# Optimization experiments

Measured on AMD Instinct MI355X. Metric: run time of the kernel, lower is better.

The kernel has to match this reference:

```python
import jax, jax.numpy as jnp
import numpy as np

B, T, D_IN, H, NH, R = 32, 1024, 64, 128, 4, 3
HD = H // NH  # 32


def _p(key, shape, scale=0.02):
    return jax.random.normal(key, shape, dtype=jnp.float32) * scale


def setup_inputs() -> dict:
    key = jax.random.key(0)
    ks = jax.random.split(key, 8)
    return {
        "x": jax.random.normal(ks[0], (B, T, D_IN), dtype=jnp.float32),
        "theta_w": _p(ks[1], (H, D_IN)),
        "theta_b": jnp.zeros((H,), jnp.float32),
        "in_proj_w": _p(ks[2], (3 * H, H)),
        "in_proj_b": jnp.zeros((3 * H,), jnp.float32),
        "out_proj_w": _p(ks[3], (H, H)),
        "out_proj_b": jnp.zeros((H,), jnp.float32),
        "ln_g": jnp.ones((H,), jnp.float32),
        "ln_b": jnp.zeros((H,), jnp.float32),
        "w1": _p(ks[4], (H, H)),
        "b1": jnp.zeros((H,), jnp.float32),
        "w2": _p(ks[5], (2, H)),
        "b2": jnp.zeros((2,), jnp.float32),
    }


def _build_adj(t, radius):
    # banded adjacency: adj[i,j] = 1/(1+|i-j|) for |i-j| <= radius, row-normalized
    idx = jnp.arange(t)
    d = jnp.abs(idx[:, None] - idx[None, :])
    adj = jnp.where(d <= radius, 1.0 / (1.0 + d.astype(jnp.float32)), 0.0)
    return adj / jnp.clip(adj.sum(axis=1, keepdims=True), 1e-8)


def reference(x, theta_w, theta_b, in_proj_w, in_proj_b, out_proj_w, out_proj_b,
              ln_g, ln_b, w1, b1, w2, b2):
    h = x @ theta_w.T + theta_b                       # [B,T,H]
    adj = _build_adj(T, R)                            # [T,T]
    g = jnp.einsum('ij,bjh->bih', adj, h)             # banded temporal aggregation

    # torch nn.MultiheadAttention (batch_first, eval -> no dropout)
    qkv = g @ in_proj_w.T + in_proj_b                 # [B,T,3H]
    q, k, v = jnp.split(qkv, 3, axis=-1)
    split_heads = lambda t: t.reshape(B, T, NH, HD).transpose(0, 2, 1, 3)
    q, k, v = split_heads(q), split_heads(k), split_heads(v)
    scores = jnp.einsum('bntd,bnsd->bnts', q, k) / jnp.sqrt(jnp.float32(HD))
    attn = jax.nn.softmax(scores, axis=-1)
    o = jnp.einsum('bnts,bnsd->bntd', attn, v)
    o = o.transpose(0, 2, 1, 3).reshape(B, T, H)
    a = o @ out_proj_w.T + out_proj_b                 # [B,T,H]

    # head on last timestep: LayerNorm -> Linear -> GELU(exact) -> Linear
    last = a[:, -1, :]                                # [B,H]
    mu = last.mean(-1, keepdims=True)
    var = ((last - mu) ** 2).mean(-1, keepdims=True)
    ln = (last - mu) / jnp.sqrt(var + 1e-5) * ln_g + ln_b
    hid = jax.nn.gelu(ln @ w1.T + b1, approximate=False)
    return hid @ w2.T + b2                            # [B,2]
```

## Files before the change

kernel.cpp:

```cpp
#include <hip/hip_runtime.h>
#include <math.h>

#define TT 1024

__global__ __launch_bounds__(256) void k_qr(
    const float* __restrict__ x, const float* __restrict__ theta_w,
    const float* __restrict__ theta_b, const float* __restrict__ ipw,
    const float* __restrict__ ipb, float* __restrict__ r_out) {
  const int b = blockIdx.x;
  const int tid = threadIdx.x;
  __shared__ float s_xs[64];
  __shared__ float s_y[128];
  __shared__ float s_q[128];
  __shared__ float s_z[4][128];
  const float* __restrict__ xb = x + (size_t)b * TT * 64;

  if (tid < 64) {
    float acc = xb[(TT - 1) * 64 + tid]
              + 0.5f        * xb[(TT - 2) * 64 + tid]
              + (1.f / 3.f) * xb[(TT - 3) * 64 + tid]
              + 0.25f       * xb[(TT - 4) * 64 + tid];
    s_xs[tid] = acc * (12.f / 25.f);
  }
  __syncthreads();
  if (tid < 128) {
    const float* tr = theta_w + tid * 64;
    float acc = theta_b[tid];
    for (int d = 0; d < 64; ++d) acc += tr[d] * s_xs[d];
    s_y[tid] = acc;
  }
  __syncthreads();
  {
    const int g = tid >> 4, l = tid & 15;
    for (int pass = 0; pass < 8; ++pass) {
      const int e = pass * 16 + g;
      const float* wr = ipw + e * 128 + l * 8;
      float acc = 0.f;
      #pragma unroll
      for (int u = 0; u < 8; ++u) acc += wr[u] * s_y[l * 8 + u];
      acc += __shfl_xor(acc, 1);
      acc += __shfl_xor(acc, 2);
      acc += __shfl_xor(acc, 4);
      acc += __shfl_xor(acc, 8);
      if (l == 0) s_q[e] = acc + ipb[e];
    }
  }
  __syncthreads();
  for (int rep = 0; rep < 2; ++rep) {
    const int idx = tid + rep * 256;
    const int n = idx >> 7, c = idx & 127;
    const float* qn = &s_q[n * 32];
    float acc = 0.f;
    for (int e = 0; e < 32; ++e) acc += ipw[(128 + n * 32 + e) * 128 + c] * qn[e];
    s_z[n][c] = acc;
  }
  __syncthreads();
  {
    const int n = tid >> 6, d = tid & 63;
    const float* zn = s_z[n];
    float acc = 0.f;
    for (int c = 0; c < 128; ++c) acc += theta_w[c * 64 + d] * zn[c];
    r_out[(b * 4 + n) * 64 + d] = acc * 0.17677669529663687f;
  }
}

__global__ __launch_bounds__(256) void k_t(
    const float* __restrict__ x, const float* __restrict__ r_in,
    float* __restrict__ t_out) {
  const int b = blockIdx.x >> 4;
  const int chunk = blockIdx.x & 15;
  const int tid = threadIdx.x;
  __shared__ __align__(16) float s_r[256];
  s_r[tid] = r_in[b * 256 + tid];
  __syncthreads();
  const int g = tid >> 4, l = tid & 15;
  const float4 r0 = ((const float4*)(s_r +   0))[l];
  const float4 r1 = ((const float4*)(s_r +  64))[l];
  const float4 r2 = ((const float4*)(s_r + 128))[l];
  const float4 r3 = ((const float4*)(s_r + 192))[l];
  const float* __restrict__ xb = x + ((size_t)b * TT + chunk * 64) * 64;
  for (int it = 0; it < 4; ++it) {
    const int jj = it * 16 + g;
    const float4 xv = ((const float4*)(xb + jj * 64))[l];
    float p0 = xv.x * r0.x + xv.y * r0.y + xv.z * r0.z + xv.w * r0.w;
    float p1 = xv.x * r1.x + xv.y * r1.y + xv.z * r1.z + xv.w * r1.w;
    float p2 = xv.x * r2.x + xv.y * r2.y + xv.z * r2.z + xv.w * r2.w;
    float p3 = xv.x * r3.x + xv.y * r3.y + xv.z * r3.z + xv.w * r3.w;
    #pragma unroll
    for (int m = 1; m <= 8; m <<= 1) {
      p0 += __shfl_xor(p0, m);
      p1 += __shfl_xor(p1, m);
      p2 += __shfl_xor(p2, m);
      p3 += __shfl_xor(p3, m);
    }
    if (l == 0) {
      const int j = chunk * 64 + jj;
      t_out[(b * 4 + 0) * TT + j] = p0;
      t_out[(b * 4 + 1) * TT + j] = p1;
      t_out[(b * 4 + 2) * TT + j] = p2;
      t_out[(b * 4 + 3) * TT + j] = p3;
    }
  }
}

__global__ __launch_bounds__(256) void k_sm(float* __restrict__ t_pt) {
  const int bn = blockIdx.x;
  const int tid = threadIdx.x;
  __shared__ __align__(16) float s_t[TT];
  __shared__ float s_p[TT];
  __shared__ float s_red[4];
  ((float4*)s_t)[tid] = ((const float4*)(t_pt + bn * TT))[tid];
  __syncthreads();

  float sc[4], wsv[4];
  float lmax = -1e30f;
  const int s0 = tid * 4;
  for (int k = 0; k < 4; ++k) {
    const int s = s0 + k;
    float acc = 0.f, wsum = 0.f;
    #pragma unroll
    for (int dj = -3; dj <= 3; ++dj) {
      const int j = s + dj;
      if (j >= 0 && j < TT) {
        const float w = 1.f / (1.f + (float)(dj < 0 ? -dj : dj));
        acc += w * s_t[j];
        wsum += w;
      }
    }
    sc[k] = acc / wsum;
    wsv[k] = wsum;
    lmax = fmaxf(lmax, sc[k]);
  }
  #pragma unroll
  for (int m = 32; m >= 1; m >>= 1) lmax = fmaxf(lmax, __shfl_xor(lmax, m));
  if ((tid & 63) == 0) s_red[tid >> 6] = lmax;
  __syncthreads();
  const float bmax = fmaxf(fmaxf(s_red[0], s_red[1]), fmaxf(s_red[2], s_red[3]));
  __syncthreads();
  float lsum = 0.f;
  for (int k = 0; k < 4; ++k) {
    const float e = expf(sc[k] - bmax);
    lsum += e;
    s_p[s0 + k] = e / wsv[k];
  }
  #pragma unroll
  for (int m = 32; m >= 1; m >>= 1) lsum += __shfl_xor(lsum, m);
  if ((tid & 63) == 0) s_red[tid >> 6] = lsum;
  __syncthreads();
  const float inv_denom = 1.f / (s_red[0] + s_red[1] + s_red[2] + s_red[3]);
  for (int k = 0; k < 4; ++k) {
    const int j = s0 + k;
    float acc = 0.f;
    #pragma unroll
    for (int dj = -3; dj <= 3; ++dj) {
      const int s = j + dj;
      if (s >= 0 && s < TT)
        acc += (1.f / (1.f + (float)(dj < 0 ? -dj : dj))) * s_p[s];
    }
    t_pt[bn * TT + j] = acc * inv_denom;
  }
}

__global__ __launch_bounds__(256) void k_u(
    const float* __restrict__ x, const float* __restrict__ pt_in,
    float* __restrict__ up_out) {
  const int b = blockIdx.x >> 4;
  const int chunk = blockIdx.x & 15;
  const int tid = threadIdx.x;
  __shared__ __align__(16) float s_x[64][64];
  __shared__ float s_p[4][64];
  const float* __restrict__ xb = x + ((size_t)b * TT + chunk * 64) * 64;
  #pragma unroll
  for (int it = 0; it < 4; ++it) {
    const int i4 = tid + it * 256;
    ((float4*)&s_x[0][0])[i4] = ((const float4*)xb)[i4];
  }
  {
    const int n = tid >> 6, jj = tid & 63;
    s_p[n][jj] = pt_in[(b * 4 + n) * TT + chunk * 64 + jj];
  }
  __syncthreads();
  const int n = tid >> 6, d = tid & 63;
  float acc = 0.f;
  for (int jj = 0; jj < 64; ++jj) acc += s_p[n][jj] * s_x[jj][d];
  up_out[((b * 16 + chunk) * 4 + n) * 64 + d] = acc;
}

__global__ __launch_bounds__(128) void k_tail(
    const float* __restrict__ up_in, const float* __restrict__ theta_w,
    const float* __restrict__ theta_b, const float* __restrict__ ipw,
    const float* __restrict__ ipb, const float* __restrict__ Wout,
    const float* __restrict__ outb, const float* __restrict__ ln_g,
    const float* __restrict__ ln_b, const float* __restrict__ w1,
    const float* __restrict__ b1, const float* __restrict__ w2,
    const float* __restrict__ b2, float* __restrict__ out) {
  const int b = blockIdx.x;
  const int tid = threadIdx.x;
  __shared__ float s_u[256];
  __shared__ float s_w[4][128];
  __shared__ float s_o[128], s_ln[128], s_hid[128], s_red[2];

  for (int rep = 0; rep < 2; ++rep) {
    const int idx = tid + rep * 128;
    float acc = 0.f;
    for (int c = 0; c < 16; ++c) acc += up_in[(b * 16 + c) * 256 + idx];
    s_u[idx] = acc;
  }
  __syncthreads();
  for (int rep = 0; rep < 4; ++rep) {
    const int idx = tid + rep * 128;
    const int n = idx >> 7, c = idx & 127;
    const float* tr = theta_w + c * 64;
    const float* un = &s_u[n * 64];
    float acc = theta_b[c];
    for (int d = 0; d < 64; ++d) acc += tr[d] * un[d];
    s_w[n][c] = acc;
  }
  __syncthreads();
  {
    const int e = tid, n = e >> 5;
    const float* wr = ipw + (256 + e) * 128;
    const float* wn = s_w[n];
    float acc = ipb[256 + e];
    for (int c = 0; c < 128; ++c) acc += wr[c] * wn[c];
    s_o[e] = acc;
  }
  __syncthreads();
  const int e = tid;
  float a = outb[e];
  {
    const float* wr = Wout + e * 128;
    for (int f = 0; f < 128; ++f) a += wr[f] * s_o[f];
  }
  float sum = a;
  #pragma unroll
  for (int m = 32; m >= 1; m >>= 1) sum += __shfl_xor(sum, m);
  if ((e & 63) == 0) s_red[e >> 6] = sum;
  __syncthreads();
  const float mu = (s_red[0] + s_red[1]) * (1.f / 128.f);
  __syncthreads();
  const float d = a - mu;
  float sq = d * d;
  #pragma unroll
  for (int m = 32; m >= 1; m >>= 1) sq += __shfl_xor(sq, m);
  if ((e & 63) == 0) s_red[e >> 6] = sq;
  __syncthreads();
  const float var = (s_red[0] + s_red[1]) * (1.f / 128.f);
  const float ln = d / sqrtf(var + 1e-5f) * ln_g[e] + ln_b[e];
  s_ln[e] = ln;
  __syncthreads();
  float h = b1[e];
  {
    const float* w1r = w1 + e * 128;
    for (int f = 0; f < 128; ++f) h += w1r[f] * s_ln[f];
  }
  h = 0.5f * h * (1.f + erff(h * 0.70710678118654752f));
  s_hid[e] = h;
  __syncthreads();
  if (e < 2) {
    float acc = b2[e];
    const float* w2r = w2 + e * 128;
    for (int f = 0; f < 128; ++f) acc += w2r[f] * s_hid[f];
    out[b * 2 + e] = acc;
  }
}

extern "C" void kernel_launch(void* const* d_in, const int* in_sizes, int n_in,
                              void* d_out, int out_size, void* d_ws, size_t ws_size,
                              hipStream_t stream) {
  const float* x       = (const float*)d_in[0];
  const float* theta_w = (const float*)d_in[1];
  const float* theta_b = (const float*)d_in[2];
  const float* ipw     = (const float*)d_in[3];
  const float* ipb     = (const float*)d_in[4];
  const float* outw    = (const float*)d_in[5];
  const float* outb    = (const float*)d_in[6];
  const float* ln_g    = (const float*)d_in[7];
  const float* ln_b    = (const float*)d_in[8];
  const float* w1      = (const float*)d_in[9];
  const float* b1      = (const float*)d_in[10];
  const float* w2      = (const float*)d_in[11];
  const float* b2      = (const float*)d_in[12];

  float* ws = (float*)d_ws;
  float* r  = ws;
  float* t  = ws + 8192;
  float* up = ws + 8192 + 131072;

  k_qr  <<< 32, 256, 0, stream>>>(x, theta_w, theta_b, ipw, ipb, r);
  k_t   <<<512, 256, 0, stream>>>(x, r, t);
  k_sm  <<<128, 256, 0, stream>>>(t);
  k_u   <<<512, 256, 0, stream>>>(x, t, up);
  k_tail<<< 32, 128, 0, stream>>>(up, theta_w, theta_b, ipw, ipb, outw, outb,
                                  ln_g, ln_b, w1, b1, w2, b2, (float*)d_out);
}
```

Measured before the change: 117.9 us.

## Fuse five-stage pipeline into one 1024-thread kernel per batch

Merges the query/r computation, score projection, banded softmax, value aggregation and MLP head into a single kernel with one 1024-thread block per batch, keeping all intermediates in shared memory. This removes four extra launches and the global-memory round trips through the workspace. The trade-off is only 32 blocks across the device, so each batch's 256 KB of x is streamed by a single CU rather than 16. Shared memory use also rises to roughly 60 KB per block.

```diff
diff --git a/kernel.cpp b/kernel.cpp
--- a/kernel.cpp
+++ b/kernel.cpp
@@ -3,191 +3,8 @@
 
 #define TT 1024
 
-__global__ __launch_bounds__(256) void k_qr(
+__global__ __launch_bounds__(1024) void k_fused(
     const float* __restrict__ x, const float* __restrict__ theta_w,
-    const float* __restrict__ theta_b, const float* __restrict__ ipw,
-    const float* __restrict__ ipb, float* __restrict__ r_out) {
-  const int b = blockIdx.x;
-  const int tid = threadIdx.x;
-  __shared__ float s_xs[64];
-  __shared__ float s_y[128];
-  __shared__ float s_q[128];
-  __shared__ float s_z[4][128];
-  const float* __restrict__ xb = x + (size_t)b * TT * 64;
-
-  if (tid < 64) {
-    float acc = xb[(TT - 1) * 64 + tid]
-              + 0.5f        * xb[(TT - 2) * 64 + tid]
-              + (1.f / 3.f) * xb[(TT - 3) * 64 + tid]
-              + 0.25f       * xb[(TT - 4) * 64 + tid];
-    s_xs[tid] = acc * (12.f / 25.f);
-  }
-  __syncthreads();
-  if (tid < 128) {
-    const float* tr = theta_w + tid * 64;
-    float acc = theta_b[tid];
-    for (int d = 0; d < 64; ++d) acc += tr[d] * s_xs[d];
-    s_y[tid] = acc;
-  }
-  __syncthreads();
-  {
-    const int g = tid >> 4, l = tid & 15;
-    for (int pass = 0; pass < 8; ++pass) {
-      const int e = pass * 16 + g;
-      const float* wr = ipw + e * 128 + l * 8;
-      float acc = 0.f;
-      #pragma unroll
-      for (int u = 0; u < 8; ++u) acc += wr[u] * s_y[l * 8 + u];
-      acc += __shfl_xor(acc, 1);
-      acc += __shfl_xor(acc, 2);
-      acc += __shfl_xor(acc, 4);
-      acc += __shfl_xor(acc, 8);
-      if (l == 0) s_q[e] = acc + ipb[e];
-    }
-  }
-  __syncthreads();
-  for (int rep = 0; rep < 2; ++rep) {
-    const int idx = tid + rep * 256;
-    const int n = idx >> 7, c = idx & 127;
-    const float* qn = &s_q[n * 32];
-    float acc = 0.f;
-    for (int e = 0; e < 32; ++e) acc += ipw[(128 + n * 32 + e) * 128 + c] * qn[e];
-    s_z[n][c] = acc;
-  }
-  __syncthreads();
-  {
-    const int n = tid >> 6, d = tid & 63;
-    const float* zn = s_z[n];
-    float acc = 0.f;
-    for (int c = 0; c < 128; ++c) acc += theta_w[c * 64 + d] * zn[c];
-    r_out[(b * 4 + n) * 64 + d] = acc * 0.17677669529663687f;
-  }
-}
-
-__global__ __launch_bounds__(256) void k_t(
-    const float* __restrict__ x, const float* __restrict__ r_in,
-    float* __restrict__ t_out) {
-  const int b = blockIdx.x >> 4;
-  const int chunk = blockIdx.x & 15;
-  const int tid = threadIdx.x;
-  __shared__ __align__(16) float s_r[256];
-  s_r[tid] = r_in[b * 256 + tid];
-  __syncthreads();
-  const int g = tid >> 4, l = tid & 15;
-  const float4 r0 = ((const float4*)(s_r +   0))[l];
-  const float4 r1 = ((const float4*)(s_r +  64))[l];
-  const float4 r2 = ((const float4*)(s_r + 128))[l];
-  const float4 r3 = ((const float4*)(s_r + 192))[l];
-  const float* __restrict__ xb = x + ((size_t)b * TT + chunk * 64) * 64;
-  for (int it = 0; it < 4; ++it) {
-    const int jj = it * 16 + g;
-    const float4 xv = ((const float4*)(xb + jj * 64))[l];
-    float p0 = xv.x * r0.x + xv.y * r0.y + xv.z * r0.z + xv.w * r0.w;
-    float p1 = xv.x * r1.x + xv.y * r1.y + xv.z * r1.z + xv.w * r1.w;
-    float p2 = xv.x * r2.x + xv.y * r2.y + xv.z * r2.z + xv.w * r2.w;
-    float p3 = xv.x * r3.x + xv.y * r3.y + xv.z * r3.z + xv.w * r3.w;
-    #pragma unroll
-    for (int m = 1; m <= 8; m <<= 1) {
-      p0 += __shfl_xor(p0, m);
-      p1 += __shfl_xor(p1, m);
-      p2 += __shfl_xor(p2, m);
-      p3 += __shfl_xor(p3, m);
-    }
-    if (l == 0) {
-      const int j = chunk * 64 + jj;
-      t_out[(b * 4 + 0) * TT + j] = p0;
-      t_out[(b * 4 + 1) * TT + j] = p1;
-      t_out[(b * 4 + 2) * TT + j] = p2;
-      t_out[(b * 4 + 3) * TT + j] = p3;
-    }
-  }
-}
-
-__global__ __launch_bounds__(256) void k_sm(float* __restrict__ t_pt) {
-  const int bn = blockIdx.x;
-  const int tid = threadIdx.x;
-  __shared__ __align__(16) float s_t[TT];
-  __shared__ float s_p[TT];
-  __shared__ float s_red[4];
-  ((float4*)s_t)[tid] = ((const float4*)(t_pt + bn * TT))[tid];
-  __syncthreads();
-
-  float sc[4], wsv[4];
-  float lmax = -1e30f;
-  const int s0 = tid * 4;
-  for (int k = 0; k < 4; ++k) {
-    const int s = s0 + k;
-    float acc = 0.f, wsum = 0.f;
-    #pragma unroll
-    for (int dj = -3; dj <= 3; ++dj) {
-      const int j = s + dj;
-      if (j >= 0 && j < TT) {
-        const float w = 1.f / (1.f + (float)(dj < 0 ? -dj : dj));
-        acc += w * s_t[j];
-        wsum += w;
-      }
-    }
-    sc[k] = acc / wsum;
-    wsv[k] = wsum;
-    lmax = fmaxf(lmax, sc[k]);
-  }
-  #pragma unroll
-  for (int m = 32; m >= 1; m >>= 1) lmax = fmaxf(lmax, __shfl_xor(lmax, m));
-  if ((tid & 63) == 0) s_red[tid >> 6] = lmax;
-  __syncthreads();
-  const float bmax = fmaxf(fmaxf(s_red[0], s_red[1]), fmaxf(s_red[2], s_red[3]));
-  __syncthreads();
-  float lsum = 0.f;
-  for (int k = 0; k < 4; ++k) {
-    const float e = expf(sc[k] - bmax);
-    lsum += e;
-    s_p[s0 + k] = e / wsv[k];
-  }
-  #pragma unroll
-  for (int m = 32; m >= 1; m >>= 1) lsum += __shfl_xor(lsum, m);
-  if ((tid & 63) == 0) s_red[tid >> 6] = lsum;
-  __syncthreads();
-  const float inv_denom = 1.f / (s_red[0] + s_red[1] + s_red[2] + s_red[3]);
-  for (int k = 0; k < 4; ++k) {
-    const int j = s0 + k;
-    float acc = 0.f;
-    #pragma unroll
-    for (int dj = -3; dj <= 3; ++dj) {
-      const int s = j + dj;
-      if (s >= 0 && s < TT)
-        acc += (1.f / (1.f + (float)(dj < 0 ? -dj : dj))) * s_p[s];
-    }
-    t_pt[bn * TT + j] = acc * inv_denom;
-  }
-}
-
-__global__ __launch_bounds__(256) void k_u(
-    const float* __restrict__ x, const float* __restrict__ pt_in,
-    float* __restrict__ up_out) {
-  const int b = blockIdx.x >> 4;
-  const int chunk = blockIdx.x & 15;
-  const int tid = threadIdx.x;
-  __shared__ __align__(16) float s_x[64][64];
-  __shared__ float s_p[4][64];
-  const float* __restrict__ xb = x + ((size_t)b * TT + chunk * 64) * 64;
-  #pragma unroll
-  for (int it = 0; it < 4; ++it) {
-    const int i4 = tid + it * 256;
-    ((float4*)&s_x[0][0])[i4] = ((const float4*)xb)[i4];
-  }
-  {
-    const int n = tid >> 6, jj = tid & 63;
-    s_p[n][jj] = pt_in[(b * 4 + n) * TT + chunk * 64 + jj];
-  }
-  __syncthreads();
-  const int n = tid >> 6, d = tid & 63;
-  float acc = 0.f;
-  for (int jj = 0; jj < 64; ++jj) acc += s_p[n][jj] * s_x[jj][d];
-  up_out[((b * 16 + chunk) * 4 + n) * 64 + d] = acc;
-}
-
-__global__ __launch_bounds__(128) void k_tail(
-    const float* __restrict__ up_in, const float* __restrict__ theta_w,
     const float* __restrict__ theta_b, const float* __restrict__ ipw,
     const float* __restrict__ ipb, const float* __restrict__ Wout,
     const float* __restrict__ outb, const float* __restrict__ ln_g,
@@ -196,20 +13,187 @@
     const float* __restrict__ b2, float* __restrict__ out) {
   const int b = blockIdx.x;
   const int tid = threadIdx.x;
+
+  __shared__ float s_xs[64];
+  __shared__ float s_y[128];
+  __shared__ float s_q[128];
+  __shared__ float s_z[4][128];
+  __shared__ __align__(16) float s_r[256];
+  __shared__ __align__(16) float s_t[4][TT];
+  __shared__ __align__(16) float s_p[4][TT];
+  __shared__ __align__(16) float s_ptT[TT][4];
+  __shared__ float s_up[16][4][64];
   __shared__ float s_u[256];
   __shared__ float s_w[4][128];
-  __shared__ float s_o[128], s_ln[128], s_hid[128], s_red[2];
-
-  for (int rep = 0; rep < 2; ++rep) {
-    const int idx = tid + rep * 128;
+  __shared__ float s_o[128], s_ln[128], s_hid[128];
+  __shared__ float s_red4[4][4];
+  __shared__ float s_red2[2];
+
+  const float* __restrict__ xb = x + (size_t)b * TT * 64;
+
+  if (tid < 64) {
+    float acc = xb[(TT - 1) * 64 + tid]
+              + 0.5f        * xb[(TT - 2) * 64 + tid]
+              + (1.f / 3.f) * xb[(TT - 3) * 64 + tid]
+              + 0.25f       * xb[(TT - 4) * 64 + tid];
+    s_xs[tid] = acc * (12.f / 25.f);
+  }
+  __syncthreads();
+  if (tid < 128) {
+    const float* tr = theta_w + tid * 64;
+    float acc = theta_b[tid];
+    for (int d = 0; d < 64; ++d) acc += tr[d] * s_xs[d];
+    s_y[tid] = acc;
+  }
+  __syncthreads();
+  if (tid < 256) {
+    const int g = tid >> 4, l = tid & 15;
+    for (int pass = 0; pass < 8; ++pass) {
+      const int e = pass * 16 + g;
+      const float* wr = ipw + e * 128 + l * 8;
+      float acc = 0.f;
+      #pragma unroll
+      for (int u = 0; u < 8; ++u) acc += wr[u] * s_y[l * 8 + u];
+      acc += __shfl_xor(acc, 1);
+      acc += __shfl_xor(acc, 2);
+      acc += __shfl_xor(acc, 4);
+      acc += __shfl_xor(acc, 8);
+      if (l == 0) s_q[e] = acc + ipb[e];
+    }
+  }
+  __syncthreads();
+  if (tid < 512) {
+    const int n = tid >> 7, c = tid & 127;
+    const float* qn = &s_q[n * 32];
     float acc = 0.f;
-    for (int c = 0; c < 16; ++c) acc += up_in[(b * 16 + c) * 256 + idx];
-    s_u[idx] = acc;
-  }
-  __syncthreads();
-  for (int rep = 0; rep < 4; ++rep) {
-    const int idx = tid + rep * 128;
-    const int n = idx >> 7, c = idx & 127;
+    for (int e = 0; e < 32; ++e) acc += ipw[(128 + n * 32 + e) * 128 + c] * qn[e];
+    s_z[n][c] = acc;
+  }
+  __syncthreads();
+  if (tid < 256) {
+    const int n = tid >> 6, d = tid & 63;
+    const float* zn = s_z[n];
+    float acc = 0.f;
+    for (int c = 0; c < 128; ++c) acc += theta_w[c * 64 + d] * zn[c];
+    s_r[n * 64 + d] = acc * 0.17677669529663687f;
+  }
+  __syncthreads();
+
+  {
+    const int g = tid >> 4, l = tid & 15;
+    const float4 r0 = ((const float4*)(s_r +   0))[l];
+    const float4 r1 = ((const float4*)(s_r +  64))[l];
+    const float4 r2 = ((const float4*)(s_r + 128))[l];
+    const float4 r3 = ((const float4*)(s_r + 192))[l];
+    for (int it = 0; it < 16; ++it) {
+      const int j = it * 64 + g;
+      const float4 xv = ((const float4*)(xb + j * 64))[l];
+      float p0 = xv.x * r0.x + xv.y * r0.y + xv.z * r0.z + xv.w * r0.w;
+      float p1 = xv.x * r1.x + xv.y * r1.y + xv.z * r1.z + xv.w * r1.w;
+      float p2 = xv.x * r2.x + xv.y * r2.y + xv.z * r2.z + xv.w * r2.w;
+      float p3 = xv.x * r3.x + xv.y * r3.y + xv.z * r3.z + xv.w * r3.w;
+      #pragma unroll
+      for (int m = 1; m <= 8; m <<= 1) {
+        p0 += __shfl_xor(p0, m);
+        p1 += __shfl_xor(p1, m);
+        p2 += __shfl_xor(p2, m);
+        p3 += __shfl_xor(p3, m);
+      }
+      if (l == 0) {
+        s_t[0][j] = p0;
+        s_t[1][j] = p1;
+        s_t[2][j] = p2;
+        s_t[3][j] = p3;
+      }
+    }
+  }
+  __syncthreads();
+
+  {
+    const int hg = tid >> 8, ht = tid & 255;
+    float sc[4], wsv[4];
+    float lmax = -1e30f;
+    #pragma unroll
+    for (int k = 0; k < 4; ++k) {
+      const int s = ht + k * 256;
+      float acc = 0.f, wsum = 0.f;
+      #pragma unroll
+      for (int dj = -3; dj <= 3; ++dj) {
+        const int j = s + dj;
+        if (j >= 0 && j < TT) {
+          const float w = 1.f / (1.f + (float)(dj < 0 ? -dj : dj));
+          acc += w * s_t[hg][j];
+          wsum += w;
+        }
+      }
+      sc[k] = acc / wsum;
+      wsv[k] = wsum;
+      lmax = fmaxf(lmax, sc[k]);
+    }
+    #pragma unroll
+    for (int m = 32; m >= 1; m >>= 1) lmax = fmaxf(lmax, __shfl_xor(lmax, m));
+    if ((ht & 63) == 0) s_red4[hg][ht >> 6] = lmax;
+    __syncthreads();
+    const float bmax = fmaxf(fmaxf(s_red4[hg][0], s_red4[hg][1]),
+                             fmaxf(s_red4[hg][2], s_red4[hg][3]));
+    __syncthreads();
+    float lsum = 0.f;
+    #pragma unroll
+    for (int k = 0; k < 4; ++k) {
+      const float e = expf(sc[k] - bmax);
+      lsum += e;
+      s_p[hg][ht + k * 256] = e / wsv[k];
+    }
+    #pragma unroll
+    for (int m = 32; m >= 1; m >>= 1) lsum += __shfl_xor(lsum, m);
+    if ((ht & 63) == 0) s_red4[hg][ht >> 6] = lsum;
+    __syncthreads();
+    const float inv_denom =
+        1.f / (s_red4[hg][0] + s_red4[hg][1] + s_red4[hg][2] + s_red4[hg][3]);
+    #pragma unroll
+    for (int k = 0; k < 4; ++k) {
+      const int j = ht + k * 256;
+      float acc = 0.f;
+      #pragma unroll
+      for (int dj = -3; dj <= 3; ++dj) {
+        const int s = j + dj;
+        if (s >= 0 && s < TT)
+          acc += (1.f / (1.f + (float)(dj < 0 ? -dj : dj))) * s_p[hg][s];
+      }
+      s_ptT[j][hg] = acc * inv_denom;
+    }
+  }
+  __syncthreads();
+
+  {
+    const int jp = tid >> 6, d = tid & 63;
+    const float* xr = xb + (size_t)(jp * 64) * 64 + d;
+    float a0 = 0.f, a1 = 0.f, a2 = 0.f, a3 = 0.f;
+    for (int jj = 0; jj < 64; ++jj) {
+      const float xv = xr[jj * 64];
+      const int j = jp * 64 + jj;
+      const float4 pv = *(const float4*)(&s_ptT[j][0]);
+      a0 += pv.x * xv;
+      a1 += pv.y * xv;
+      a2 += pv.z * xv;
+      a3 += pv.w * xv;
+    }
+    s_up[jp][0][d] = a0;
+    s_up[jp][1][d] = a1;
+    s_up[jp][2][d] = a2;
+    s_up[jp][3][d] = a3;
+  }
+  __syncthreads();
+  if (tid < 256) {
+    const int n = tid >> 6, d = tid & 63;
+    float acc = 0.f;
+    for (int c = 0; c < 16; ++c) acc += s_up[c][n][d];
+    s_u[n * 64 + d] = acc;
+  }
+  __syncthreads();
+
+  if (tid < 512) {
+    const int n = tid >> 7, c = tid & 127;
     const float* tr = theta_w + c * 64;
     const float* un = &s_u[n * 64];
     float acc = theta_b[c];
@@ -217,7 +201,7 @@
     s_w[n][c] = acc;
   }
   __syncthreads();
-  {
+  if (tid < 128) {
     const int e = tid, n = e >> 5;
     const float* wr = ipw + (256 + e) * 128;
     const float* wn = s_w[n];
@@ -226,42 +210,50 @@
     s_o[e] = acc;
   }
   __syncthreads();
-  const int e = tid;
-  float a = outb[e];
-  {
+  float a_val = 0.f;
+  if (tid < 128) {
+    const int e = tid;
+    a_val = outb[e];
     const float* wr = Wout + e * 128;
-    for (int f = 0; f < 128; ++f) a += wr[f] * s_o[f];
-  }
-  float sum = a;
-  #pragma unroll
-  for (int m = 32; m >= 1; m >>= 1) sum += __shfl_xor(sum, m);
-  if ((e & 63) == 0) s_red[e >> 6] = sum;
-  __syncthreads();
-  const float mu = (s_red[0] + s_red[1]) * (1.f / 128.f);
-  __syncthreads();
-  const float d = a - mu;
-  float sq = d * d;
-  #pragma unroll
-  for (int m = 32; m >= 1; m >>= 1) sq += __shfl_xor(sq, m);
-  if ((e & 63) == 0) s_red[e >> 6] = sq;
-  __syncthreads();
-  const float var = (s_red[0] + s_red[1]) * (1.f / 128.f);
-  const float ln = d / sqrtf(var + 1e-5f) * ln_g[e] + ln_b[e];
-  s_ln[e] = ln;
-  __syncthreads();
-  float h = b1[e];
-  {
+    for (int f = 0; f < 128; ++f) a_val += wr[f] * s_o[f];
+    float sum = a_val;
+    #pragma unroll
+    for (int m = 32; m >= 1; m >>= 1) sum += __shfl_xor(sum, m);
+    if ((e & 63) == 0) s_red2[e >> 6] = sum;
+  }
+  __syncthreads();
+  const float mu = (s_red2[0] + s_red2[1]) * (1.f / 128.f);
+  __syncthreads();
+  if (tid < 128) {
+    const float d = a_val - mu;
+    float sq = d * d;
+    #pragma unroll
+    for (int m = 32; m >= 1; m >>= 1) sq += __shfl_xor(sq, m);
+    if ((tid & 63) == 0) s_red2[tid >> 6] = sq;
+  }
+  __syncthreads();
+  if (tid < 128) {
+    const int e = tid;
+    const float var = (s_red2[0] + s_red2[1]) * (1.f / 128.f);
+    const float d = a_val - mu;
+    const float ln = d / sqrtf(var + 1e-5f) * ln_g[e] + ln_b[e];
+    s_ln[e] = ln;
+  }
+  __syncthreads();
+  if (tid < 128) {
+    const int e = tid;
+    float h = b1[e];
     const float* w1r = w1 + e * 128;
     for (int f = 0; f < 128; ++f) h += w1r[f] * s_ln[f];
-  }
-  h = 0.5f * h * (1.f + erff(h * 0.70710678118654752f));
-  s_hid[e] = h;
-  __syncthreads();
-  if (e < 2) {
-    float acc = b2[e];
-    const float* w2r = w2 + e * 128;
+    h = 0.5f * h * (1.f + erff(h * 0.70710678118654752f));
+    s_hid[e] = h;
+  }
+  __syncthreads();
+  if (tid < 2) {
+    float acc = b2[tid];
+    const float* w2r = w2 + tid * 128;
     for (int f = 0; f < 128; ++f) acc += w2r[f] * s_hid[f];
-    out[b * 2 + e] = acc;
+    out[b * 2 + tid] = acc;
   }
 }
 
@@ -282,15 +274,8 @@
   const float* w2      = (const float*)d_in[11];
   const float* b2      = (const float*)d_in[12];
 
-  float* ws = (float*)d_ws;
-  float* r  = ws;
-  float* t  = ws + 8192;
-  float* up = ws + 8192 + 131072;
-
-  k_qr  <<< 32, 256, 0, stream>>>(x, theta_w, theta_b, ipw, ipb, r);
-  k_t   <<<512, 256, 0, stream>>>(x, r, t);
-  k_sm  <<<128, 256, 0, stream>>>(t);
-  k_u   <<<512, 256, 0, stream>>>(x, t, up);
-  k_tail<<< 32, 128, 0, stream>>>(up, theta_w, theta_b, ipw, ipb, outw, outb,
-                                  ln_g, ln_b, w1, b1, w2, b2, (float*)d_out);
+  (void)d_ws; (void)ws_size;
+
+  k_fused<<<32, 1024, 0, stream>>>(x, theta_w, theta_b, ipw, ipb, outw, outb,
+                                   ln_g, ln_b, w1, b1, w2, b2, (float*)d_out);
 }
```

Measured after the change: 118.2 us. Within noise of the previous version (+0.3%).

## Fuse qr, scoring, softmax and value-aggregation kernels into one per-(batch,head) block

Applied to the files above, without the earlier changes.

Replaces four kernels (k_qr, k_t, k_sm, k_u) with a single 1024-thread kernel, one block per (batch, head). Each block computes its head's query projection, the scores, the banded softmax and the weighted x reduction entirely in shared memory. This removes three launches and the global round-trips for r, t and the partial up sums. In exchange each block re-reads x for its batch (four times per batch overall), recomputes the shared prefix per head, and the grid shrinks to 128 blocks.

```diff
diff --git a/kernel.cpp b/kernel.cpp
--- a/kernel.cpp
+++ b/kernel.cpp
@@ -3,16 +3,26 @@
 
 #define TT 1024
 
-__global__ __launch_bounds__(256) void k_qr(
+__global__ __launch_bounds__(1024) void k_bn(
     const float* __restrict__ x, const float* __restrict__ theta_w,
     const float* __restrict__ theta_b, const float* __restrict__ ipw,
-    const float* __restrict__ ipb, float* __restrict__ r_out) {
-  const int b = blockIdx.x;
+    const float* __restrict__ ipb, float* __restrict__ u_ws) {
+  const int bid = blockIdx.x;
+  const int b = bid & 31;
+  const int n = bid >> 5;
   const int tid = threadIdx.x;
+
   __shared__ float s_xs[64];
   __shared__ float s_y[128];
-  __shared__ float s_q[128];
-  __shared__ float s_z[4][128];
+  __shared__ float s_qn[32];
+  __shared__ float s_z[128];
+  __shared__ __align__(16) float s_r[64];
+  __shared__ __align__(16) float s_t[TT];
+  __shared__ __align__(16) float s_p[TT];
+  __shared__ __align__(16) float s_pt[TT];
+  __shared__ float s_up[16][64];
+  __shared__ float s_red[16];
+
   const float* __restrict__ xb = x + (size_t)b * TT * 64;
 
   if (tid < 64) {
@@ -30,164 +40,113 @@
     s_y[tid] = acc;
   }
   __syncthreads();
-  {
+  if (tid < 512) {
     const int g = tid >> 4, l = tid & 15;
-    for (int pass = 0; pass < 8; ++pass) {
-      const int e = pass * 16 + g;
-      const float* wr = ipw + e * 128 + l * 8;
-      float acc = 0.f;
+    const int e = n * 32 + g;
+    const float* wr = ipw + e * 128 + l * 8;
+    float acc = 0.f;
+    #pragma unroll
+    for (int u = 0; u < 8; ++u) acc += wr[u] * s_y[l * 8 + u];
+    acc += __shfl_xor(acc, 1);
+    acc += __shfl_xor(acc, 2);
+    acc += __shfl_xor(acc, 4);
+    acc += __shfl_xor(acc, 8);
+    if (l == 0) s_qn[g] = acc + ipb[e];
+  }
+  __syncthreads();
+  if (tid < 128) {
+    const int c = tid;
+    float acc = 0.f;
+    for (int e = 0; e < 32; ++e)
+      acc += ipw[(128 + n * 32 + e) * 128 + c] * s_qn[e];
+    s_z[c] = acc;
+  }
+  __syncthreads();
+  if (tid < 64) {
+    const int d = tid;
+    float acc = 0.f;
+    for (int c = 0; c < 128; ++c) acc += theta_w[c * 64 + d] * s_z[c];
+    s_r[d] = acc * 0.17677669529663687f;
+  }
+  __syncthreads();
+
+  {
+    const int g = tid >> 4, l = tid & 15;
+    const float4 rv = ((const float4*)s_r)[l];
+    for (int it = 0; it < 16; ++it) {
+      const int j = it * 64 + g;
+      const float4 xv = ((const float4*)(xb + j * 64))[l];
+      float p = xv.x * rv.x + xv.y * rv.y + xv.z * rv.z + xv.w * rv.w;
       #pragma unroll
-      for (int u = 0; u < 8; ++u) acc += wr[u] * s_y[l * 8 + u];
-      acc += __shfl_xor(acc, 1);
-      acc += __shfl_xor(acc, 2);
-      acc += __shfl_xor(acc, 4);
-      acc += __shfl_xor(acc, 8);
-      if (l == 0) s_q[e] = acc + ipb[e];
+      for (int m = 1; m <= 8; m <<= 1) p += __shfl_xor(p, m);
+      if (l == 0) s_t[j] = p;
     }
   }
   __syncthreads();
-  for (int rep = 0; rep < 2; ++rep) {
-    const int idx = tid + rep * 256;
-    const int n = idx >> 7, c = idx & 127;
-    const float* qn = &s_q[n * 32];
-    float acc = 0.f;
-    for (int e = 0; e < 32; ++e) acc += ipw[(128 + n * 32 + e) * 128 + c] * qn[e];
-    s_z[n][c] = acc;
-  }
-  __syncthreads();
-  {
-    const int n = tid >> 6, d = tid & 63;
-    const float* zn = s_z[n];
-    float acc = 0.f;
-    for (int c = 0; c < 128; ++c) acc += theta_w[c * 64 + d] * zn[c];
-    r_out[(b * 4 + n) * 64 + d] = acc * 0.17677669529663687f;
-  }
-}
-
-__global__ __launch_bounds__(256) void k_t(
-    const float* __restrict__ x, const float* __restrict__ r_in,
-    float* __restrict__ t_out) {
-  const int b = blockIdx.x >> 4;
-  const int chunk = blockIdx.x & 15;
-  const int tid = threadIdx.x;
-  __shared__ __align__(16) float s_r[256];
-  s_r[tid] = r_in[b * 256 + tid];
-  __syncthreads();
-  const int g = tid >> 4, l = tid & 15;
-  const float4 r0 = ((const float4*)(s_r +   0))[l];
-  const float4 r1 = ((const float4*)(s_r +  64))[l];
-  const float4 r2 = ((const float4*)(s_r + 128))[l];
-  const float4 r3 = ((const float4*)(s_r + 192))[l];
-  const float* __restrict__ xb = x + ((size_t)b * TT + chunk * 64) * 64;
-  for (int it = 0; it < 4; ++it) {
-    const int jj = it * 16 + g;
-    const float4 xv = ((const float4*)(xb + jj * 64))[l];
-    float p0 = xv.x * r0.x + xv.y * r0.y + xv.z * r0.z + xv.w * r0.w;
-    float p1 = xv.x * r1.x + xv.y * r1.y + xv.z * r1.z + xv.w * r1.w;
-    float p2 = xv.x * r2.x + xv.y * r2.y + xv.z * r2.z + xv.w * r2.w;
-    float p3 = xv.x * r3.x + xv.y * r3.y + xv.z * r3.z + xv.w * r3.w;
-    #pragma unroll
-    for (int m = 1; m <= 8; m <<= 1) {
-      p0 += __shfl_xor(p0, m);
-      p1 += __shfl_xor(p1, m);
-      p2 += __shfl_xor(p2, m);
-      p3 += __shfl_xor(p3, m);
-    }
-    if (l == 0) {
-      const int j = chunk * 64 + jj;
-      t_out[(b * 4 + 0) * TT + j] = p0;
-      t_out[(b * 4 + 1) * TT + j] = p1;
-      t_out[(b * 4 + 2) * TT + j] = p2;
-      t_out[(b * 4 + 3) * TT + j] = p3;
-    }
-  }
-}
-
-__global__ __launch_bounds__(256) void k_sm(float* __restrict__ t_pt) {
-  const int bn = blockIdx.x;
-  const int tid = threadIdx.x;
-  __shared__ __align__(16) float s_t[TT];
-  __shared__ float s_p[TT];
-  __shared__ float s_red[4];
-  ((float4*)s_t)[tid] = ((const float4*)(t_pt + bn * TT))[tid];
-  __syncthreads();
-
-  float sc[4], wsv[4];
-  float lmax = -1e30f;
-  const int s0 = tid * 4;
-  for (int k = 0; k < 4; ++k) {
-    const int s = s0 + k;
+
+  {
+    const int j = tid;
     float acc = 0.f, wsum = 0.f;
     #pragma unroll
     for (int dj = -3; dj <= 3; ++dj) {
-      const int j = s + dj;
-      if (j >= 0 && j < TT) {
+      const int jj = j + dj;
+      if (jj >= 0 && jj < TT) {
         const float w = 1.f / (1.f + (float)(dj < 0 ? -dj : dj));
-        acc += w * s_t[j];
+        acc += w * s_t[jj];
         wsum += w;
       }
     }
-    sc[k] = acc / wsum;
-    wsv[k] = wsum;
-    lmax = fmaxf(lmax, sc[k]);
-  }
-  #pragma unroll
-  for (int m = 32; m >= 1; m >>= 1) lmax = fmaxf(lmax, __shfl_xor(lmax, m));
-  if ((tid & 63) == 0) s_red[tid >> 6] = lmax;
-  __syncthreads();
-  const float bmax = fmaxf(fmaxf(s_red[0], s_red[1]), fmaxf(s_red[2], s_red[3]));
-  __syncthreads();
-  float lsum = 0.f;
-  for (int k = 0; k < 4; ++k) {
-    const float e = expf(sc[k] - bmax);
-    lsum += e;
-    s_p[s0 + k] = e / wsv[k];
-  }
-  #pragma unroll
-  for (int m = 32; m >= 1; m >>= 1) lsum += __shfl_xor(lsum, m);
-  if ((tid & 63) == 0) s_red[tid >> 6] = lsum;
-  __syncthreads();
-  const float inv_denom = 1.f / (s_red[0] + s_red[1] + s_red[2] + s_red[3]);
-  for (int k = 0; k < 4; ++k) {
-    const int j = s0 + k;
-    float acc = 0.f;
+    const float sc = acc / wsum;
+    float lmax = sc;
+    #pragma unroll
+    for (int m = 32; m >= 1; m >>= 1) lmax = fmaxf(lmax, __shfl_xor(lmax, m));
+    if ((tid & 63) == 0) s_red[tid >> 6] = lmax;
+    __syncthreads();
+    float bmax = -1e30f;
+    #pragma unroll
+    for (int w = 0; w < 16; ++w) bmax = fmaxf(bmax, s_red[w]);
+    __syncthreads();
+    const float e = expf(sc - bmax);
+    s_p[j] = e / wsum;
+    float lsum = e;
+    #pragma unroll
+    for (int m = 32; m >= 1; m >>= 1) lsum += __shfl_xor(lsum, m);
+    if ((tid & 63) == 0) s_red[tid >> 6] = lsum;
+    __syncthreads();
+    float tsum = 0.f;
+    #pragma unroll
+    for (int w = 0; w < 16; ++w) tsum += s_red[w];
+    const float inv_denom = 1.f / tsum;
+    float acc2 = 0.f;
     #pragma unroll
     for (int dj = -3; dj <= 3; ++dj) {
       const int s = j + dj;
       if (s >= 0 && s < TT)
-        acc += (1.f / (1.f + (float)(dj < 0 ? -dj : dj))) * s_p[s];
+        acc2 += (1.f / (1.f + (float)(dj < 0 ? -dj : dj))) * s_p[s];
     }
-    t_pt[bn * TT + j] = acc * inv_denom;
+    s_pt[j] = acc2 * inv_denom;
+  }
+  __syncthreads();
+
+  {
+    const int jp = tid >> 6, d = tid & 63;
+    const float* xr = xb + (size_t)(jp * 64) * 64 + d;
+    float acc = 0.f;
+    for (int jj = 0; jj < 64; ++jj)
+      acc += s_pt[jp * 64 + jj] * xr[jj * 64];
+    s_up[jp][d] = acc;
+  }
+  __syncthreads();
+  if (tid < 64) {
+    const int d = tid;
+    float acc = 0.f;
+    for (int c = 0; c < 16; ++c) acc += s_up[c][d];
+    u_ws[((size_t)b * 4 + n) * 64 + d] = acc;
   }
 }
 
-__global__ __launch_bounds__(256) void k_u(
-    const float* __restrict__ x, const float* __restrict__ pt_in,
-    float* __restrict__ up_out) {
-  const int b = blockIdx.x >> 4;
-  const int chunk = blockIdx.x & 15;
-  const int tid = threadIdx.x;
-  __shared__ __align__(16) float s_x[64][64];
-  __shared__ float s_p[4][64];
-  const float* __restrict__ xb = x + ((size_t)b * TT + chunk * 64) * 64;
-  #pragma unroll
-  for (int it = 0; it < 4; ++it) {
-    const int i4 = tid + it * 256;
-    ((float4*)&s_x[0][0])[i4] = ((const float4*)xb)[i4];
-  }
-  {
-    const int n = tid >> 6, jj = tid & 63;
-    s_p[n][jj] = pt_in[(b * 4 + n) * TT + chunk * 64 + jj];
-  }
-  __syncthreads();
-  const int n = tid >> 6, d = tid & 63;
-  float acc = 0.f;
-  for (int jj = 0; jj < 64; ++jj) acc += s_p[n][jj] * s_x[jj][d];
-  up_out[((b * 16 + chunk) * 4 + n) * 64 + d] = acc;
-}
-
 __global__ __launch_bounds__(128) void k_tail(
-    const float* __restrict__ up_in, const float* __restrict__ theta_w,
+    const float* __restrict__ u_in, const float* __restrict__ theta_w,
     const float* __restrict__ theta_b, const float* __restrict__ ipw,
     const float* __restrict__ ipb, const float* __restrict__ Wout,
     const float* __restrict__ outb, const float* __restrict__ ln_g,
@@ -202,9 +161,7 @@
 
   for (int rep = 0; rep < 2; ++rep) {
     const int idx = tid + rep * 128;
-    float acc = 0.f;
-    for (int c = 0; c < 16; ++c) acc += up_in[(b * 16 + c) * 256 + idx];
-    s_u[idx] = acc;
+    s_u[idx] = u_in[b * 256 + idx];
   }
   __syncthreads();
   for (int rep = 0; rep < 4; ++rep) {
@@ -282,15 +239,9 @@
   const float* w2      = (const float*)d_in[11];
   const float* b2      = (const float*)d_in[12];
 
-  float* ws = (float*)d_ws;
-  float* r  = ws;
-  float* t  = ws + 8192;
-  float* up = ws + 8192 + 131072;
-
-  k_qr  <<< 32, 256, 0, stream>>>(x, theta_w, theta_b, ipw, ipb, r);
-  k_t   <<<512, 256, 0, stream>>>(x, r, t);
-  k_sm  <<<128, 256, 0, stream>>>(t);
-  k_u   <<<512, 256, 0, stream>>>(x, t, up);
-  k_tail<<< 32, 128, 0, stream>>>(up, theta_w, theta_b, ipw, ipb, outw, outb,
-                                  ln_g, ln_b, w1, b1, w2, b2, (float*)d_out);
+  float* u_ws = (float*)d_ws;
+
+  k_bn  <<<128, 1024, 0, stream>>>(x, theta_w, theta_b, ipw, ipb, u_ws);
+  k_tail<<< 32,  128, 0, stream>>>(u_ws, theta_w, theta_b, ipw, ipb, outw, outb,
+                                   ln_g, ln_b, w1, b1, w2, b2, (float*)d_out);
 }
```

After: 112.3 us. -4.7%, faster.
